# Kernel optimization log

Hardware: AMD Instinct MI355X
Metric: run time of the kernel (lower is better)

The kernel has to match this reference:

```python
import jax, jax.numpy as jnp
import numpy as np

N_NODES, BATCH, VOCAB, HID, OUT = 2047, 128, 32, 128, 128


def setup_inputs() -> dict:
    key = jax.random.key(0)
    ks = jax.random.split(key, 18)
    w = 0.05  # small init scale (xavier-ish for these sizes)
    rn = lambda k, s, sc=w: jax.random.normal(k, s, dtype=jnp.float32) * sc
    return {
        "targets": jax.random.normal(ks[0], (N_NODES, BATCH, VOCAB), dtype=jnp.float32),
        "masks": jnp.ones((N_NODES, BATCH), dtype=jnp.float32),
        "wir_w": rn(ks[1], (HID, VOCAB)), "wir_b": rn(ks[2], (HID,)),
        "whr_w": rn(ks[3], (HID, 2 * HID)), "whr_b": rn(ks[4], (HID,)),
        "wiz_w": rn(ks[5], (HID, VOCAB)), "wiz_b": rn(ks[6], (HID,)),
        "whz_w": rn(ks[7], (HID, 2 * HID)), "whz_b": rn(ks[8], (HID,)),
        "win_w": rn(ks[9], (HID, VOCAB)), "win_b": rn(ks[10], (HID,)),
        "whn_w": rn(ks[11], (HID, 2 * HID)), "whn_b": rn(ks[12], (HID,)),
        "mu_w": rn(ks[13], (OUT, HID)), "mu_b": rn(ks[14], (OUT,)),
        "lv_w": rn(ks[15], (OUT, HID)), "lv_b": rn(ks[16], (OUT,)),
    }


def _encode(targets, masks, wir_w, wir_b, whr_w, whr_b, wiz_w, wiz_b,
            whz_w, whz_b, win_w, win_b, whn_w, whn_b):
    # Complete binary tree in heap layout: level d occupies nodes [2^d-1, 2^(d+1)-1).
    # Bottom-up level sweep == the original node-by-node recursion, but each
    # level's GRU221 cells are batched into one fused GEMM group.
    Nn, B, V = targets.shape
    H = wir_w.shape[0]
    D = int(np.log2(Nn + 1))  # static at trace time
    h_prev = None  # hidden states of the level below, [2^(d+1)*B, H]
    for d in range(D - 1, -1, -1):
        n = 1 << d
        start = n - 1
        x = targets[start:start + n].reshape(n * B, V)
        m = masks[start:start + n].reshape(n * B, 1)
        if h_prev is None:  # leaves: zero children
            h1 = jnp.zeros((n * B, H), dtype=targets.dtype)
            h2 = h1
        else:
            hp = h_prev.reshape(2 * n, B, H)
            h1 = hp[0::2].reshape(n * B, H)  # left children (heap idx 2i+1)
            h2 = hp[1::2].reshape(n * B, H)  # right children (heap idx 2i+2)
        h = jnp.concatenate([h1, h2], axis=1)  # [nB, 2H]
        r = jax.nn.sigmoid(x @ wir_w.T + wir_b + h @ whr_w.T + whr_b)
        z = jax.nn.sigmoid(x @ wiz_w.T + wiz_b + h @ whz_w.T + whz_b)
        c = jnp.tanh(x @ win_w.T + win_b + r * (h @ whn_w.T + whn_b))
        h_out = (1 - z) * c + z * 0.5 * h1 + z * 0.5 * h2
        h_prev = h_out * m
    return h_prev  # root hidden, [B, H]


def reference(targets, masks, wir_w, wir_b, whr_w, whr_b, wiz_w, wiz_b,
              whz_w, whz_b, win_w, win_b, whn_w, whn_b,
              mu_w, mu_b, lv_w, lv_b):
    root = _encode(targets, masks, wir_w, wir_b, whr_w, whr_b,
                   wiz_w, wiz_b, whz_w, whz_b, win_w, win_b, whn_w, whn_b)
    mu = root @ mu_w.T + mu_b
    logvar = root @ lv_w.T + lv_b
    return mu, logvar
```

## Files before the change

### kernel.cpp

```cpp
#include <hip/hip_runtime.h>
#include <hip/hip_bf16.h>
#include <math.h>

#define B 128
#define V 32
#define H 128
#define LDH 264
#define NTHR 256

typedef __attribute__((ext_vector_type(8))) short bf16x8;
typedef __attribute__((ext_vector_type(4))) float f32x4;

__device__ inline f32x4 mfma_bf16(bf16x8 a, bf16x8 b, f32x4 c) {
    return __builtin_amdgcn_mfma_f32_16x16x32_bf16(a, b, c, 0, 0, 0);
}
__device__ inline unsigned short f2bf(float f) {
    __hip_bfloat16 h = __float2bfloat16(f);
    return __builtin_bit_cast(unsigned short, h);
}
__device__ inline float bf2f(unsigned short u) {
    unsigned int x = ((unsigned int)u) << 16;
    return __builtin_bit_cast(float, x);
}
__device__ inline float fast_sigmoid(float x) {
    float e = __builtin_amdgcn_exp2f(x * -1.44269504f);
    return __builtin_amdgcn_rcpf(1.f + e);
}
__device__ inline float fast_tanh(float x) {
    float e = __builtin_amdgcn_exp2f(x * 2.88539008f);
    return 1.f - 2.f * __builtin_amdgcn_rcpf(e + 1.f);
}
__device__ inline bf16x8 load_xfrag(const float* p) {
    float4 a = *(const float4*)p;
    float4 b = *(const float4*)(p + 4);
    bf16x8 r;
    r[0] = (short)f2bf(a.x); r[1] = (short)f2bf(a.y);
    r[2] = (short)f2bf(a.z); r[3] = (short)f2bf(a.w);
    r[4] = (short)f2bf(b.x); r[5] = (short)f2bf(b.y);
    r[6] = (short)f2bf(b.z); r[7] = (short)f2bf(b.w);
    return r;
}

__global__ void prep_pack(const float* __restrict__ wir_w, const float* __restrict__ whr_w,
                          const float* __restrict__ wiz_w, const float* __restrict__ whz_w,
                          const float* __restrict__ win_w, const float* __restrict__ whn_w,
                          const float* __restrict__ wir_b, const float* __restrict__ whr_b,
                          const float* __restrict__ wiz_b, const float* __restrict__ whz_b,
                          const float* __restrict__ win_b, const float* __restrict__ whn_b,
                          const float* __restrict__ mu_w, const float* __restrict__ mu_b,
                          const float* __restrict__ lv_w, const float* __restrict__ lv_b,
                          unsigned short* __restrict__ wFrag, unsigned short* __restrict__ pFrag,
                          float* __restrict__ bias)
{
    int idx = blockIdx.x * blockDim.x + threadIdx.x;
    if (idx < 13824) {
        int lane = idx & 63;
        int ctks = idx >> 6;
        int ct = ctks % 24;
        int ks = ctks / 24;
        int g = ct >> 3;
        int t = ct & 7;
        int u = t * 16 + (lane & 15);
        const float* wi = (g == 0) ? wir_w : (g == 1) ? wiz_w : win_w;
        const float* wh = (g == 0) ? whr_w : (g == 1) ? whz_w : whn_w;
        unsigned short v[8] __attribute__((aligned(16)));
        #pragma unroll
        for (int i = 0; i < 8; ++i) {
            float f;
            if (ks == 0) { int k = 8 * (lane >> 4) + i; f = wi[u * V + k]; }
            else         { int k = (ks - 1) * 32 + 8 * (lane >> 4) + i; f = wh[u * 256 + k]; }
            v[i] = f2bf(f);
        }
        *(int4*)(wFrag + (size_t)idx * 8) = *(const int4*)v;
    } else if (idx < 13824 + 4096) {
        int pidx = idx - 13824;
        int lane = pidx & 63;
        int rest = pidx >> 6;
        int ct2 = rest & 15;
        int ks = rest >> 4;
        int sel = ct2 >> 3, tl = ct2 & 7;
        int u = tl * 16 + (lane & 15);
        const float* wsrc = sel ? lv_w : mu_w;
        unsigned short v[8] __attribute__((aligned(16)));
        #pragma unroll
        for (int i = 0; i < 8; ++i) {
            int k = ks * 32 + 8 * (lane >> 4) + i;
            v[i] = f2bf(wsrc[u * H + k]);
        }
        *(int4*)(pFrag + (size_t)pidx * 8) = *(const int4*)v;
    }
    if (idx < 6 * H) {
        int s = idx / H, u = idx % H;
        float val;
        if (s == 0)      val = wir_b[u] + whr_b[u];
        else if (s == 1) val = wiz_b[u] + whz_b[u];
        else if (s == 2) val = win_b[u];
        else if (s == 3) val = whn_b[u];
        else if (s == 4) val = mu_b[u];
        else             val = lv_b[u];
        bias[idx] = val;
    }
}

__global__ __launch_bounds__(NTHR, 4) void leaf_d9_kernel(
    const float* __restrict__ targets, const float* __restrict__ masks,
    unsigned short* __restrict__ lvl9,
    const unsigned short* __restrict__ wFrag, const float* __restrict__ bias)
{
    __shared__ __attribute__((aligned(16))) unsigned short h_lds[32 * LDH];

    const int tid = threadIdx.x;
    const int lane = tid & 63;
    const int w = tid >> 6;
    const int l15 = lane & 15;
    const int lg = lane >> 4;
    const int j = blockIdx.x >> 2;
    const int q = blockIdx.x & 3;

    const size_t r9 = (size_t)(511 + j) * B + (size_t)q * 32;
    bf16x8 x9_0 = load_xfrag(targets + (r9 + l15) * V + 8 * lg);
    bf16x8 x9_1 = load_xfrag(targets + (r9 + 16 + l15) * V + 8 * lg);

    #pragma unroll
    for (int c = 0; c < 2; ++c) {
        const size_t crow = (size_t)(1023 + 2 * j + c) * B + (size_t)q * 32;
        bf16x8 xf0 = load_xfrag(targets + (crow + l15) * V + 8 * lg);
        bf16x8 xf1 = load_xfrag(targets + (crow + 16 + l15) * V + 8 * lg);
        f32x4 z4 = {0.f, 0.f, 0.f, 0.f};
        f32x4 ar[2][2], az[2][2], an[2][2];
        #pragma unroll
        for (int rt = 0; rt < 2; ++rt)
            #pragma unroll
            for (int t = 0; t < 2; ++t) { ar[rt][t] = z4; az[rt][t] = z4; an[rt][t] = z4; }
        #pragma unroll
        for (int t = 0; t < 2; ++t) {
            int tt = 2 * w + t;
            bf16x8 br_ = *(const bf16x8*)(wFrag + ((size_t)(tt) * 64 + lane) * 8);
            bf16x8 bz_ = *(const bf16x8*)(wFrag + ((size_t)(8 + tt) * 64 + lane) * 8);
            bf16x8 bn_ = *(const bf16x8*)(wFrag + ((size_t)(16 + tt) * 64 + lane) * 8);
            ar[0][t] = mfma_bf16(xf0, br_, ar[0][t]);
            ar[1][t] = mfma_bf16(xf1, br_, ar[1][t]);
            az[0][t] = mfma_bf16(xf0, bz_, az[0][t]);
            az[1][t] = mfma_bf16(xf1, bz_, az[1][t]);
            an[0][t] = mfma_bf16(xf0, bn_, an[0][t]);
            an[1][t] = mfma_bf16(xf1, bn_, an[1][t]);
        }
        #pragma unroll
        for (int t = 0; t < 2; ++t) {
            int u = w * 32 + t * 16 + l15;
            float br = bias[u], bz = bias[128 + u], bin = bias[256 + u], bhn = bias[384 + u];
            #pragma unroll
            for (int rt = 0; rt < 2; ++rt) {
                float4 mv = *(const float4*)(masks + crow + rt * 16 + lg * 4);
                const float* mp = (const float*)&mv;
                #pragma unroll
                for (int reg = 0; reg < 4; ++reg) {
                    int row = rt * 16 + lg * 4 + reg;
                    float rg = fast_sigmoid(ar[rt][t][reg] + br);
                    float zg = fast_sigmoid(az[rt][t][reg] + bz);
                    float cg = fast_tanh(an[rt][t][reg] + bin + rg * bhn);
                    float ho = (1.f - zg) * cg;
                    h_lds[row * LDH + c * 128 + u] = f2bf(ho * mp[reg]);
                }
            }
        }
    }
    __syncthreads();

    f32x4 z4 = {0.f, 0.f, 0.f, 0.f};
    f32x4 acc_r[2][2], acc_z[2][2], acc_in[2][2], acc_hn[2][2];
    #pragma unroll
    for (int rt = 0; rt < 2; ++rt)
        #pragma unroll
        for (int t = 0; t < 2; ++t) {
            acc_r[rt][t] = z4; acc_z[rt][t] = z4; acc_in[rt][t] = z4; acc_hn[rt][t] = z4;
        }
    #pragma unroll
    for (int t = 0; t < 2; ++t) {
        int tt = 2 * w + t;
        bf16x8 br_ = *(const bf16x8*)(wFrag + ((size_t)(tt) * 64 + lane) * 8);
        bf16x8 bz_ = *(const bf16x8*)(wFrag + ((size_t)(8 + tt) * 64 + lane) * 8);
        bf16x8 bn_ = *(const bf16x8*)(wFrag + ((size_t)(16 + tt) * 64 + lane) * 8);
        acc_r[0][t] = mfma_bf16(x9_0, br_, acc_r[0][t]);
        acc_r[1][t] = mfma_bf16(x9_1, br_, acc_r[1][t]);
        acc_z[0][t] = mfma_bf16(x9_0, bz_, acc_z[0][t]);
        acc_z[1][t] = mfma_bf16(x9_1, bz_, acc_z[1][t]);
        acc_in[0][t] = mfma_bf16(x9_0, bn_, acc_in[0][t]);
        acc_in[1][t] = mfma_bf16(x9_1, bn_, acc_in[1][t]);
    }
    #pragma unroll 2
    for (int ks = 1; ks <= 8; ++ks) {
        bf16x8 a0 = *(const bf16x8*)(&h_lds[l15 * LDH + (ks - 1) * 32 + 8 * lg]);
        bf16x8 a1 = *(const bf16x8*)(&h_lds[(16 + l15) * LDH + (ks - 1) * 32 + 8 * lg]);
        size_t fb = (size_t)ks * 24 * 64;
        #pragma unroll
        for (int t = 0; t < 2; ++t) {
            int tt = 2 * w + t;
            bf16x8 br_ = *(const bf16x8*)(wFrag + (fb + (size_t)(tt) * 64 + lane) * 8);
            bf16x8 bz_ = *(const bf16x8*)(wFrag + (fb + (size_t)(8 + tt) * 64 + lane) * 8);
            bf16x8 bn_ = *(const bf16x8*)(wFrag + (fb + (size_t)(16 + tt) * 64 + lane) * 8);
            acc_r[0][t] = mfma_bf16(a0, br_, acc_r[0][t]);
            acc_r[1][t] = mfma_bf16(a1, br_, acc_r[1][t]);
            acc_z[0][t] = mfma_bf16(a0, bz_, acc_z[0][t]);
            acc_z[1][t] = mfma_bf16(a1, bz_, acc_z[1][t]);
            acc_hn[0][t] = mfma_bf16(a0, bn_, acc_hn[0][t]);
            acc_hn[1][t] = mfma_bf16(a1, bn_, acc_hn[1][t]);
        }
    }
    #pragma unroll
    for (int t = 0; t < 2; ++t) {
        int u = w * 32 + t * 16 + l15;
        float br = bias[u], bz = bias[128 + u], bin = bias[256 + u], bhn = bias[384 + u];
        #pragma unroll
        for (int rt = 0; rt < 2; ++rt) {
            float4 mv = *(const float4*)(masks + r9 + rt * 16 + lg * 4);
            const float* mp = (const float*)&mv;
            #pragma unroll
            for (int reg = 0; reg < 4; ++reg) {
                int row = rt * 16 + lg * 4 + reg;
                float rg = fast_sigmoid(acc_r[rt][t][reg] + br);
                float zg = fast_sigmoid(acc_z[rt][t][reg] + bz);
                float cg = fast_tanh(acc_in[rt][t][reg] + bin + rg * (acc_hn[rt][t][reg] + bhn));
                float h1 = bf2f(h_lds[row * LDH + u]);
                float h2 = bf2f(h_lds[row * LDH + 128 + u]);
                float ho = (1.f - zg) * cg + zg * 0.5f * (h1 + h2);
                lvl9[((size_t)j * B + (size_t)q * 32 + row) * H + u] = f2bf(ho * mp[reg]);
            }
        }
    }
}

__global__ __launch_bounds__(NTHR, 4) void level_kernel(
    const float* __restrict__ targets, const float* __restrict__ masks,
    int start,
    const unsigned short* __restrict__ prev, unsigned short* __restrict__ outb,
    const unsigned short* __restrict__ wFrag, const float* __restrict__ bias)
{
    __shared__ __attribute__((aligned(16))) unsigned short h_lds[32 * LDH];

    const int tid = threadIdx.x;
    const int lane = tid & 63;
    const int w = tid >> 6;
// ... 1 lines not shown
    const int lg = lane >> 4;
    const int n = blockIdx.x >> 2;
    const int q = blockIdx.x & 3;

    #pragma unroll
    for (int t = 0; t < 4; ++t) {
        int task = t * NTHR + tid;
        int row = task >> 5;
        int ck = task & 31;
        int4 v = *(const int4*)(prev + (((size_t)(2 * n + (ck >> 4))) * B + (size_t)q * 32 + row) * H + (ck & 15) * 8);
        *(int4*)(&h_lds[row * LDH + ck * 8]) = v;
    }
    const size_t rx = (size_t)(start + n) * B + (size_t)q * 32;
    bf16x8 x0 = load_xfrag(targets + (rx + l15) * V + 8 * lg);
    bf16x8 x1 = load_xfrag(targets + (rx + 16 + l15) * V + 8 * lg);
    __syncthreads();

    f32x4 z4 = {0.f, 0.f, 0.f, 0.f};
    f32x4 acc_r[2][2], acc_z[2][2], acc_in[2][2], acc_hn[2][2];
    #pragma unroll
    for (int rt = 0; rt < 2; ++rt)
        #pragma unroll
        for (int t = 0; t < 2; ++t) {
            acc_r[rt][t] = z4; acc_z[rt][t] = z4; acc_in[rt][t] = z4; acc_hn[rt][t] = z4;
        }
    #pragma unroll
    for (int t = 0; t < 2; ++t) {
        int tt = 2 * w + t;
        bf16x8 br_ = *(const bf16x8*)(wFrag + ((size_t)(tt) * 64 + lane) * 8);
        bf16x8 bz_ = *(const bf16x8*)(wFrag + ((size_t)(8 + tt) * 64 + lane) * 8);
        bf16x8 bn_ = *(const bf16x8*)(wFrag + ((size_t)(16 + tt) * 64 + lane) * 8);
        acc_r[0][t] = mfma_bf16(x0, br_, acc_r[0][t]);
        acc_r[1][t] = mfma_bf16(x1, br_, acc_r[1][t]);
        acc_z[0][t] = mfma_bf16(x0, bz_, acc_z[0][t]);
        acc_z[1][t] = mfma_bf16(x1, bz_, acc_z[1][t]);
        acc_in[0][t] = mfma_bf16(x0, bn_, acc_in[0][t]);
        acc_in[1][t] = mfma_bf16(x1, bn_, acc_in[1][t]);
    }
    #pragma unroll 2
    for (int ks = 1; ks <= 8; ++ks) {
        bf16x8 a0 = *(const bf16x8*)(&h_lds[l15 * LDH + (ks - 1) * 32 + 8 * lg]);
        bf16x8 a1 = *(const bf16x8*)(&h_lds[(16 + l15) * LDH + (ks - 1) * 32 + 8 * lg]);
        size_t fb = (size_t)ks * 24 * 64;
        #pragma unroll
        for (int t = 0; t < 2; ++t) {
            int tt = 2 * w + t;
            bf16x8 br_ = *(const bf16x8*)(wFrag + (fb + (size_t)(tt) * 64 + lane) * 8);
            bf16x8 bz_ = *(const bf16x8*)(wFrag + (fb + (size_t)(8 + tt) * 64 + lane) * 8);
            bf16x8 bn_ = *(const bf16x8*)(wFrag + (fb + (size_t)(16 + tt) * 64 + lane) * 8);
            acc_r[0][t] = mfma_bf16(a0, br_, acc_r[0][t]);
            acc_r[1][t] = mfma_bf16(a1, br_, acc_r[1][t]);
            acc_z[0][t] = mfma_bf16(a0, bz_, acc_z[0][t]);
            acc_z[1][t] = mfma_bf16(a1, bz_, acc_z[1][t]);
            acc_hn[0][t] = mfma_bf16(a0, bn_, acc_hn[0][t]);
            acc_hn[1][t] = mfma_bf16(a1, bn_, acc_hn[1][t]);
        }
    }
    #pragma unroll
    for (int t = 0; t < 2; ++t) {
        int u = w * 32 + t * 16 + l15;
        float br = bias[u], bz = bias[128 + u], bin = bias[256 + u], bhn = bias[384 + u];
        #pragma unroll
        for (int rt = 0; rt < 2; ++rt) {
            float4 mv = *(const float4*)(masks + rx + rt * 16 + lg * 4);
            const float* mp = (const float*)&mv;
            #pragma unroll
            for (int reg = 0; reg < 4; ++reg) {
                int row = rt * 16 + lg * 4 + reg;
                float rg = fast_sigmoid(acc_r[rt][t][reg] + br);
                float zg = fast_sigmoid(acc_z[rt][t][reg] + bz);
                float cg = fast_tanh(acc_in[rt][t][reg] + bin + rg * (acc_hn[rt][t][reg] + bhn));
                float h1 = bf2f(h_lds[row * LDH + u]);
                float h2 = bf2f(h_lds[row * LDH + 128 + u]);
                float ho = (1.f - zg) * cg + zg * 0.5f * (h1 + h2);
                outb[((size_t)n * B + (size_t)q * 32 + row) * H + u] = f2bf(ho * mp[reg]);
            }
        }
    }
}

__global__ __launch_bounds__(NTHR, 4) void pair_kernel(
    const float* __restrict__ targets, const float* __restrict__ masks,
    int du,
    const unsigned short* __restrict__ prev,
    unsigned short* __restrict__ outl,
    const unsigned short* __restrict__ wFrag, const float* __restrict__ bias,
    int do_proj, const unsigned short* __restrict__ pFrag, float* __restrict__ proj_out)
{
    __shared__ __attribute__((aligned(16))) unsigned short hc[32 * LDH];
    __shared__ __attribute__((aligned(16))) unsigned short hp[16 * LDH];

// ... 8 lines not shown

    #pragma unroll
    for (int t = 0; t < 4; ++t) {
        int task = t * NTHR + tid;
        int row = task >> 5;
        int ck = task & 31;
        int gnode = 4 * p + ((row >> 4) << 1) + (ck >> 4);
        int4 v = *(const int4*)(prev + (((size_t)gnode) * B + (size_t)c8 * 16 + (row & 15)) * H + (ck & 15) * 8);
        *(int4*)(&hc[row * LDH + ck * 8]) = v;
    }
    const size_t cbase = (size_t)((1 << du) - 1) + 2 * p;
    bf16x8 xc0 = load_xfrag(targets + ((cbase) * B + (size_t)c8 * 16 + l15) * V + 8 * lg);
    bf16x8 xc1 = load_xfrag(targets + ((cbase + 1) * B + (size_t)c8 * 16 + l15) * V + 8 * lg);
    const size_t pnode = (size_t)((1 << dl) - 1) + p;
    bf16x8 xp = load_xfrag(targets + (pnode * B + (size_t)c8 * 16 + l15) * V + 8 * lg);
    __syncthreads();

    {
        f32x4 z4 = {0.f, 0.f, 0.f, 0.f};
        f32x4 acc_r[2][2], acc_z[2][2], acc_in[2][2], acc_hn[2][2];
        #pragma unroll
        for (int rt = 0; rt < 2; ++rt)
            #pragma unroll
            for (int t = 0; t < 2; ++t) {
                acc_r[rt][t] = z4; acc_z[rt][t] = z4; acc_in[rt][t] = z4; acc_hn[rt][t] = z4;
            }
        #pragma unroll
        for (int t = 0; t < 2; ++t) {
            int tt = 2 * w + t;
            bf16x8 br_ = *(const bf16x8*)(wFrag + ((size_t)(tt) * 64 + lane) * 8);
            bf16x8 bz_ = *(const bf16x8*)(wFrag + ((size_t)(8 + tt) * 64 + lane) * 8);
            bf16x8 bn_ = *(const bf16x8*)(wFrag + ((size_t)(16 + tt) * 64 + lane) * 8);
            acc_r[0][t] = mfma_bf16(xc0, br_, acc_r[0][t]);
            acc_r[1][t] = mfma_bf16(xc1, br_, acc_r[1][t]);
            acc_z[0][t] = mfma_bf16(xc0, bz_, acc_z[0][t]);
            acc_z[1][t] = mfma_bf16(xc1, bz_, acc_z[1][t]);
            acc_in[0][t] = mfma_bf16(xc0, bn_, acc_in[0][t]);
            acc_in[1][t] = mfma_bf16(xc1, bn_, acc_in[1][t]);
        }
        #pragma unroll 2
        for (int ks = 1; ks <= 8; ++ks) {
            bf16x8 a0 = *(const bf16x8*)(&hc[l15 * LDH + (ks - 1) * 32 + 8 * lg]);
            bf16x8 a1 = *(const bf16x8*)(&hc[(16 + l15) * LDH + (ks - 1) * 32 + 8 * lg]);
            size_t fb = (size_t)ks * 24 * 64;
            #pragma unroll
            for (int t = 0; t < 2; ++t) {
                int tt = 2 * w + t;
                bf16x8 br_ = *(const bf16x8*)(wFrag + (fb + (size_t)(tt) * 64 + lane) * 8);
                bf16x8 bz_ = *(const bf16x8*)(wFrag + (fb + (size_t)(8 + tt) * 64 + lane) * 8);
                bf16x8 bn_ = *(const bf16x8*)(wFrag + (fb + (size_t)(16 + tt) * 64 + lane) * 8);
                acc_r[0][t] = mfma_bf16(a0, br_, acc_r[0][t]);
                acc_r[1][t] = mfma_bf16(a1, br_, acc_r[1][t]);
                acc_z[0][t] = mfma_bf16(a0, bz_, acc_z[0][t]);
                acc_z[1][t] = mfma_bf16(a1, bz_, acc_z[1][t]);
                acc_hn[0][t] = mfma_bf16(a0, bn_, acc_hn[0][t]);
                acc_hn[1][t] = mfma_bf16(a1, bn_, acc_hn[1][t]);
            }
        }
        #pragma unroll
        for (int t = 0; t < 2; ++t) {
            int u = w * 32 + t * 16 + l15;
            float br = bias[u], bz = bias[128 + u], bin = bias[256 + u], bhn = bias[384 + u];
            #pragma unroll
            for (int rt = 0; rt < 2; ++rt) {
                float4 mv = *(const float4*)(masks + (cbase + rt) * B + (size_t)c8 * 16 + lg * 4);
                const float* mp = (const float*)&mv;
                #pragma unroll
                for (int reg = 0; reg < 4; ++reg) {
                    int rowl = lg * 4 + reg;
                    int row = rt * 16 + rowl;
                    float rg = fast_sigmoid(acc_r[rt][t][reg] + br);
                    float zg = fast_sigmoid(acc_z[rt][t][reg] + bz);
                    float cg = fast_tanh(acc_in[rt][t][reg] + bin + rg * (acc_hn[rt][t][reg] + bhn));
                    float h1 = bf2f(hc[row * LDH + u]);
                    float h2 = bf2f(hc[row * LDH + 128 + u]);
                    float ho = (1.f - zg) * cg + zg * 0.5f * (h1 + h2);
                    hp[rowl * LDH + rt * 128 + u] = f2bf(ho * mp[reg]);
                }
            }
        }
    }
    __syncthreads();

    {
        f32x4 z4 = {0.f, 0.f, 0.f, 0.f};
        f32x4 acc_r[2], acc_z[2], acc_in[2], acc_hn[2];
        #pragma unroll
        for (int t = 0; t < 2; ++t) { acc_r[t] = z4; acc_z[t] = z4; acc_in[t] = z4; acc_hn[t] = z4; }
        #pragma unroll
        for (int t = 0; t < 2; ++t) {
            int tt = 2 * w + t;
            bf16x8 br_ = *(const bf16x8*)(wFrag + ((size_t)(tt) * 64 + lane) * 8);
            bf16x8 bz_ = *(const bf16x8*)(wFrag + ((size_t)(8 + tt) * 64 + lane) * 8);
            bf16x8 bn_ = *(const bf16x8*)(wFrag + ((size_t)(16 + tt) * 64 + lane) * 8);
            acc_r[t] = mfma_bf16(xp, br_, acc_r[t]);
            acc_z[t] = mfma_bf16(xp, bz_, acc_z[t]);
            acc_in[t] = mfma_bf16(xp, bn_, acc_in[t]);
        }
        #pragma unroll 2
        for (int ks = 1; ks <= 8; ++ks) {
            bf16x8 a = *(const bf16x8*)(&hp[l15 * LDH + (ks - 1) * 32 + 8 * lg]);
            size_t fb = (size_t)ks * 24 * 64;
            #pragma unroll
            for (int t = 0; t < 2; ++t) {
                int tt = 2 * w + t;
                bf16x8 br_ = *(const bf16x8*)(wFrag + (fb + (size_t)(tt) * 64 + lane) * 8);
                bf16x8 bz_ = *(const bf16x8*)(wFrag + (fb + (size_t)(8 + tt) * 64 + lane) * 8);
                bf16x8 bn_ = *(const bf16x8*)(wFrag + (fb + (size_t)(16 + tt) * 64 + lane) * 8);
                acc_r[t] = mfma_bf16(a, br_, acc_r[t]);
                acc_z[t] = mfma_bf16(a, bz_, acc_z[t]);
                acc_hn[t] = mfma_bf16(a, bn_, acc_hn[t]);
            }
        }
        #pragma unroll
        for (int t = 0; t < 2; ++t) {
            int u = w * 32 + t * 16 + l15;
            float br = bias[u], bz = bias[128 + u], bin = bias[256 + u], bhn = bias[384 + u];
            float4 mv = *(const float4*)(masks + pnode * B + (size_t)c8 * 16 + lg * 4);
            const float* mp = (const float*)&mv;
            #pragma unroll
            for (int reg = 0; reg < 4; ++reg) {
                int rowl = lg * 4 + reg;
                float rg = fast_sigmoid(acc_r[t][reg] + br);
                float zg = fast_sigmoid(acc_z[t][reg] + bz);
                float cg = fast_tanh(acc_in[t][reg] + bin + rg * (acc_hn[t][reg] + bhn));
                float h1 = bf2f(hp[rowl * LDH + u]);
                float h2 = bf2f(hp[rowl * LDH + 128 + u]);
                float ho = (1.f - zg) * cg + zg * 0.5f * (h1 + h2);
                unsigned short hb = f2bf(ho * mp[reg]);
                outl[((size_t)p * B + (size_t)c8 * 16 + rowl) * H + u] = hb;
                if (do_proj) hp[rowl * LDH + u] = hb;
            }
        }
    }

    if (do_proj) {
        __syncthreads();
        f32x4 z4 = {0.f, 0.f, 0.f, 0.f};
        f32x4 pa[4] = {z4, z4, z4, z4};
        #pragma unroll
        for (int ks = 0; ks < 4; ++ks) {
            bf16x8 a = *(const bf16x8*)(&hp[l15 * LDH + ks * 32 + 8 * lg]);
            #pragma unroll
            for (int jj = 0; jj < 4; ++jj) {
                bf16x8 f = *(const bf16x8*)(pFrag + (((size_t)ks * 16 + 4 * w + jj) * 64 + lane) * 8);
                pa[jj] = mfma_bf16(a, f, pa[jj]);
            }
        }
        #pragma unroll
        for (int jj = 0; jj < 4; ++jj) {
            int ct2 = 4 * w + jj;
            int sel = ct2 >> 3, tl = ct2 & 7;
            int u = tl * 16 + l15;
            float bb = bias[512 + sel * 128 + u];
            #pragma unroll
            for (int reg = 0; reg < 4; ++reg) {
                int row = c8 * 16 + lg * 4 + reg;
                proj_out[((size_t)sel * B + row) * H + u] = pa[jj][reg] + bb;
            }
        }
    }
}

extern "C" void kernel_launch(void* const* d_in, const int* in_sizes, int n_in,
                              void* d_out, int out_size, void* d_ws, size_t ws_size,
                              hipStream_t stream)
{
    const float* targets = (const float*)d_in[0];
    const float* masks   = (const float*)d_in[1];
    const float* wir_w = (const float*)d_in[2];  const float* wir_b = (const float*)d_in[3];
    const float* whr_w = (const float*)d_in[4];  const float* whr_b = (const float*)d_in[5];
    const float* wiz_w = (const float*)d_in[6];  const float* wiz_b = (const float*)d_in[7];
    const float* whz_w = (const float*)d_in[8];  const float* whz_b = (const float*)d_in[9];
    const float* win_w = (const float*)d_in[10]; const float* win_b = (const float*)d_in[11];
// ... 34 lines not shown
```

Measured before the change: 131.6 us.

## Swap MFMA operands so outputs are row-contiguous; fold bias and exp scales into weights

Swaps the A and B operands of every MFMA so each lane's four accumulator registers hold four consecutive hidden units of one batch row. This turns scalar 2-byte LDS and global stores into packed 8-byte stores, and lets biases load as float4 and seed the accumulators. The log2e scaling for sigmoid and tanh is premultiplied into the bf16 weights and biases in the prep kernel, which removes per-element multiplies and bias adds in the gate epilogues. The leaf kernel also hoists its input weight fragments into registers, at the cost of higher register pressure and a slightly different bf16 rounding of the scaled weights.

```diff
diff --git a/kernel.cpp b/kernel.cpp
--- a/kernel.cpp
+++ b/kernel.cpp
@@ -11,8 +11,8 @@
 typedef __attribute__((ext_vector_type(8))) short bf16x8;
 typedef __attribute__((ext_vector_type(4))) float f32x4;
 
-__device__ inline f32x4 mfma_bf16(bf16x8 a, bf16x8 b, f32x4 c) {
-    return __builtin_amdgcn_mfma_f32_16x16x32_bf16(a, b, c, 0, 0, 0);
+__device__ inline f32x4 mfma_wx(bf16x8 wf, bf16x8 xf, f32x4 c) {
+    return __builtin_amdgcn_mfma_f32_16x16x32_bf16(wf, xf, c, 0, 0, 0);
 }
 __device__ inline unsigned short f2bf(float f) {
     __hip_bfloat16 h = __float2bfloat16(f);
@@ -22,13 +22,11 @@
     unsigned int x = ((unsigned int)u) << 16;
     return __builtin_bit_cast(float, x);
 }
-__device__ inline float fast_sigmoid(float x) {
-    float e = __builtin_amdgcn_exp2f(x * -1.44269504f);
-    return __builtin_amdgcn_rcpf(1.f + e);
-}
-__device__ inline float fast_tanh(float x) {
-    float e = __builtin_amdgcn_exp2f(x * 2.88539008f);
-    return 1.f - 2.f * __builtin_amdgcn_rcpf(e + 1.f);
+__device__ inline float sig_pre(float y) {
+    return __builtin_amdgcn_rcpf(1.f + __builtin_amdgcn_exp2f(y));
+}
+__device__ inline float tanh_pre(float y) {
+    return 1.f - 2.f * __builtin_amdgcn_rcpf(__builtin_amdgcn_exp2f(y) + 1.f);
 }
 __device__ inline bf16x8 load_xfrag(const float* p) {
     float4 a = *(const float4*)p;
@@ -38,6 +36,12 @@
     r[2] = (short)f2bf(a.z); r[3] = (short)f2bf(a.w);
     r[4] = (short)f2bf(b.x); r[5] = (short)f2bf(b.y);
     r[6] = (short)f2bf(b.z); r[7] = (short)f2bf(b.w);
+    return r;
+}
+__device__ inline uint2 pack4(float a, float b, float c, float d) {
+    uint2 r;
+    r.x = (unsigned int)f2bf(a) | ((unsigned int)f2bf(b) << 16);
+    r.y = (unsigned int)f2bf(c) | ((unsigned int)f2bf(d) << 16);
     return r;
 }
 
@@ -61,6 +65,7 @@
         int g = ct >> 3;
         int t = ct & 7;
         int u = t * 16 + (lane & 15);
+        const float scl = (g == 2) ? 2.88539008f : -1.44269504f;
         const float* wi = (g == 0) ? wir_w : (g == 1) ? wiz_w : win_w;
         const float* wh = (g == 0) ? whr_w : (g == 1) ? whz_w : whn_w;
         unsigned short v[8] __attribute__((aligned(16)));
@@ -69,7 +74,7 @@
             float f;
             if (ks == 0) { int k = 8 * (lane >> 4) + i; f = wi[u * V + k]; }
             else         { int k = (ks - 1) * 32 + 8 * (lane >> 4) + i; f = wh[u * 256 + k]; }
-            v[i] = f2bf(f);
+            v[i] = f2bf(f * scl);
         }
         *(int4*)(wFrag + (size_t)idx * 8) = *(const int4*)v;
     } else if (idx < 13824 + 4096) {
@@ -92,10 +97,10 @@
     if (idx < 6 * H) {
         int s = idx / H, u = idx % H;
         float val;
-        if (s == 0)      val = wir_b[u] + whr_b[u];
-        else if (s == 1) val = wiz_b[u] + whz_b[u];
-        else if (s == 2) val = win_b[u];
-        else if (s == 3) val = whn_b[u];
+        if (s == 0)      val = (wir_b[u] + whr_b[u]) * -1.44269504f;
+        else if (s == 1) val = (wiz_b[u] + whz_b[u]) * -1.44269504f;
+        else if (s == 2) val = win_b[u] * 2.88539008f;
+        else if (s == 3) val = whn_b[u] * 2.88539008f;
         else if (s == 4) val = mu_b[u];
         else             val = lv_b[u];
         bias[idx] = val;
@@ -117,6 +122,23 @@
     const int j = blockIdx.x >> 2;
     const int q = blockIdx.x & 3;
 
+    bf16x8 w0[2][3];
+    #pragma unroll
+    for (int t = 0; t < 2; ++t)
+        #pragma unroll
+        for (int g = 0; g < 3; ++g)
+            w0[t][g] = *(const bf16x8*)(wFrag + (((size_t)g * 8 + 2 * w + t) * 64 + lane) * 8);
+
+    f32x4 b_r[2], b_z[2], b_in[2], b_hn[2];
+    #pragma unroll
+    for (int t = 0; t < 2; ++t) {
+        int u0 = w * 32 + t * 16 + lg * 4;
+        b_r[t]  = *(const f32x4*)(bias + u0);
+        b_z[t]  = *(const f32x4*)(bias + 128 + u0);
+        b_in[t] = *(const f32x4*)(bias + 256 + u0);
+        b_hn[t] = *(const f32x4*)(bias + 384 + u0);
+    }
+
     const size_t r9 = (size_t)(511 + j) * B + (size_t)q * 32;
     bf16x8 x9_0 = load_xfrag(targets + (r9 + l15) * V + 8 * lg);
     bf16x8 x9_1 = load_xfrag(targets + (r9 + 16 + l15) * V + 8 * lg);
@@ -126,67 +148,59 @@
         const size_t crow = (size_t)(1023 + 2 * j + c) * B + (size_t)q * 32;
         bf16x8 xf0 = load_xfrag(targets + (crow + l15) * V + 8 * lg);
         bf16x8 xf1 = load_xfrag(targets + (crow + 16 + l15) * V + 8 * lg);
-        f32x4 z4 = {0.f, 0.f, 0.f, 0.f};
         f32x4 ar[2][2], az[2][2], an[2][2];
         #pragma unroll
-        for (int rt = 0; rt < 2; ++rt)
-            #pragma unroll
-            for (int t = 0; t < 2; ++t) { ar[rt][t] = z4; az[rt][t] = z4; an[rt][t] = z4; }
-        #pragma unroll
-        for (int t = 0; t < 2; ++t) {
-            int tt = 2 * w + t;
-            bf16x8 br_ = *(const bf16x8*)(wFrag + ((size_t)(tt) * 64 + lane) * 8);
-            bf16x8 bz_ = *(const bf16x8*)(wFrag + ((size_t)(8 + tt) * 64 + lane) * 8);
-            bf16x8 bn_ = *(const bf16x8*)(wFrag + ((size_t)(16 + tt) * 64 + lane) * 8);
-            ar[0][t] = mfma_bf16(xf0, br_, ar[0][t]);
-            ar[1][t] = mfma_bf16(xf1, br_, ar[1][t]);
-            az[0][t] = mfma_bf16(xf0, bz_, az[0][t]);
-            az[1][t] = mfma_bf16(xf1, bz_, az[1][t]);
-            an[0][t] = mfma_bf16(xf0, bn_, an[0][t]);
-            an[1][t] = mfma_bf16(xf1, bn_, an[1][t]);
-        }
-        #pragma unroll
-        for (int t = 0; t < 2; ++t) {
-            int u = w * 32 + t * 16 + l15;
-            float br = bias[u], bz = bias[128 + u], bin = bias[256 + u], bhn = bias[384 + u];
-            #pragma unroll
-            for (int rt = 0; rt < 2; ++rt) {
-                float4 mv = *(const float4*)(masks + crow + rt * 16 + lg * 4);
-                const float* mp = (const float*)&mv;
+        for (int t = 0; t < 2; ++t) {
+            ar[0][t] = b_r[t];  ar[1][t] = b_r[t];
+            az[0][t] = b_z[t];  az[1][t] = b_z[t];
+            an[0][t] = b_in[t]; an[1][t] = b_in[t];
+        }
+        #pragma unroll
+        for (int t = 0; t < 2; ++t) {
+            ar[0][t] = mfma_wx(w0[t][0], xf0, ar[0][t]);
+            ar[1][t] = mfma_wx(w0[t][0], xf1, ar[1][t]);
+            az[0][t] = mfma_wx(w0[t][1], xf0, az[0][t]);
+            az[1][t] = mfma_wx(w0[t][1], xf1, az[1][t]);
+            an[0][t] = mfma_wx(w0[t][2], xf0, an[0][t]);
+            an[1][t] = mfma_wx(w0[t][2], xf1, an[1][t]);
+        }
+        #pragma unroll
+        for (int rt = 0; rt < 2; ++rt) {
+            int row = rt * 16 + l15;
+            float m = masks[crow + row];
+            #pragma unroll
+            for (int t = 0; t < 2; ++t) {
+                int u0 = w * 32 + t * 16 + lg * 4;
+                float ho[4];
                 #pragma unroll
                 for (int reg = 0; reg < 4; ++reg) {
-                    int row = rt * 16 + lg * 4 + reg;
-                    float rg = fast_sigmoid(ar[rt][t][reg] + br);
-                    float zg = fast_sigmoid(az[rt][t][reg] + bz);
-                    float cg = fast_tanh(an[rt][t][reg] + bin + rg * bhn);
-                    float ho = (1.f - zg) * cg;
-                    h_lds[row * LDH + c * 128 + u] = f2bf(ho * mp[reg]);
+                    float rg = sig_pre(ar[rt][t][reg]);
+                    float zg = sig_pre(az[rt][t][reg]);
+                    float cg = tanh_pre(an[rt][t][reg] + rg * b_hn[t][reg]);
+                    ho[reg] = (cg - zg * cg) * m;
                 }
+                *(uint2*)(&h_lds[row * LDH + c * 128 + u0]) = pack4(ho[0], ho[1], ho[2], ho[3]);
             }
         }
     }
     __syncthreads();
 
-    f32x4 z4 = {0.f, 0.f, 0.f, 0.f};
     f32x4 acc_r[2][2], acc_z[2][2], acc_in[2][2], acc_hn[2][2];
     #pragma unroll
-    for (int rt = 0; rt < 2; ++rt)
-        #pragma unroll
-        for (int t = 0; t < 2; ++t) {
-            acc_r[rt][t] = z4; acc_z[rt][t] = z4; acc_in[rt][t] = z4; acc_hn[rt][t] = z4;
-        }
-    #pragma unroll
-    for (int t = 0; t < 2; ++t) {
-        int tt = 2 * w + t;
-        bf16x8 br_ = *(const bf16x8*)(wFrag + ((size_t)(tt) * 64 + lane) * 8);
-        bf16x8 bz_ = *(const bf16x8*)(wFrag + ((size_t)(8 + tt) * 64 + lane) * 8);
-        bf16x8 bn_ = *(const bf16x8*)(wFrag + ((size_t)(16 + tt) * 64 + lane) * 8);
-        acc_r[0][t] = mfma_bf16(x9_0, br_, acc_r[0][t]);
-        acc_r[1][t] = mfma_bf16(x9_1, br_, acc_r[1][t]);
-        acc_z[0][t] = mfma_bf16(x9_0, bz_, acc_z[0][t]);
-        acc_z[1][t] = mfma_bf16(x9_1, bz_, acc_z[1][t]);
-        acc_in[0][t] = mfma_bf16(x9_0, bn_, acc_in[0][t]);
-        acc_in[1][t] = mfma_bf16(x9_1, bn_, acc_in[1][t]);
+    for (int t = 0; t < 2; ++t) {
+        acc_r[0][t] = b_r[t];   acc_r[1][t] = b_r[t];
+        acc_z[0][t] = b_z[t];   acc_z[1][t] = b_z[t];
+        acc_in[0][t] = b_in[t]; acc_in[1][t] = b_in[t];
+        acc_hn[0][t] = b_hn[t]; acc_hn[1][t] = b_hn[t];
+    }
+    #pragma unroll
+    for (int t = 0; t < 2; ++t) {
+        acc_r[0][t] = mfma_wx(w0[t][0], x9_0, acc_r[0][t]);
+        acc_r[1][t] = mfma_wx(w0[t][0], x9_1, acc_r[1][t]);
+        acc_z[0][t] = mfma_wx(w0[t][1], x9_0, acc_z[0][t]);
+        acc_z[1][t] = mfma_wx(w0[t][1], x9_1, acc_z[1][t]);
+        acc_in[0][t] = mfma_wx(w0[t][2], x9_0, acc_in[0][t]);
+        acc_in[1][t] = mfma_wx(w0[t][2], x9_1, acc_in[1][t]);
     }
     #pragma unroll 2
     for (int ks = 1; ks <= 8; ++ks) {
@@ -196,36 +210,39 @@
         #pragma unroll
         for (int t = 0; t < 2; ++t) {
             int tt = 2 * w + t;
-            bf16x8 br_ = *(const bf16x8*)(wFrag + (fb + (size_t)(tt) * 64 + lane) * 8);
-            bf16x8 bz_ = *(const bf16x8*)(wFrag + (fb + (size_t)(8 + tt) * 64 + lane) * 8);
-            bf16x8 bn_ = *(const bf16x8*)(wFrag + (fb + (size_t)(16 + tt) * 64 + lane) * 8);
-            acc_r[0][t] = mfma_bf16(a0, br_, acc_r[0][t]);
-            acc_r[1][t] = mfma_bf16(a1, br_, acc_r[1][t]);
-            acc_z[0][t] = mfma_bf16(a0, bz_, acc_z[0][t]);
-            acc_z[1][t] = mfma_bf16(a1, bz_, acc_z[1][t]);
-            acc_hn[0][t] = mfma_bf16(a0, bn_, acc_hn[0][t]);
-            acc_hn[1][t] = mfma_bf16(a1, bn_, acc_hn[1][t]);
-        }
-    }
-    #pragma unroll
-    for (int t = 0; t < 2; ++t) {
-        int u = w * 32 + t * 16 + l15;
-        float br = bias[u], bz = bias[128 + u], bin = bias[256 + u], bhn = bias[384 + u];
-        #pragma unroll
-        for (int rt = 0; rt < 2; ++rt) {
-            float4 mv = *(const float4*)(masks + r9 + rt * 16 + lg * 4);
-            const float* mp = (const float*)&mv;
+            bf16x8 wr_ = *(const bf16x8*)(wFrag + (fb + (size_t)(tt) * 64 + lane) * 8);
+            bf16x8 wz_ = *(const bf16x8*)(wFrag + (fb + (size_t)(8 + tt) * 64 + lane) * 8);
+            bf16x8 wn_ = *(const bf16x8*)(wFrag + (fb + (size_t)(16 + tt) * 64 + lane) * 8);
+            acc_r[0][t] = mfma_wx(wr_, a0, acc_r[0][t]);
+            acc_r[1][t] = mfma_wx(wr_, a1, acc_r[1][t]);
+            acc_z[0][t] = mfma_wx(wz_, a0, acc_z[0][t]);
+            acc_z[1][t] = mfma_wx(wz_, a1, acc_z[1][t]);
+            acc_hn[0][t] = mfma_wx(wn_, a0, acc_hn[0][t]);
+            acc_hn[1][t] = mfma_wx(wn_, a1, acc_hn[1][t]);
+        }
+    }
+    #pragma unroll
+    for (int rt = 0; rt < 2; ++rt) {
+        int row = rt * 16 + l15;
+        float m = masks[r9 + row];
+        #pragma unroll
+        for (int t = 0; t < 2; ++t) {
+            int u0 = w * 32 + t * 16 + lg * 4;
+            ushort4 h1v = *(const ushort4*)(&h_lds[row * LDH + u0]);
+            ushort4 h2v = *(const ushort4*)(&h_lds[row * LDH + 128 + u0]);
+            const unsigned short* h1p = (const unsigned short*)&h1v;
+            const unsigned short* h2p = (const unsigned short*)&h2v;
+            float ho[4];
             #pragma unroll
             for (int reg = 0; reg < 4; ++reg) {
-                int row = rt * 16 + lg * 4 + reg;
-                float rg = fast_sigmoid(acc_r[rt][t][reg] + br);
-                float zg = fast_sigmoid(acc_z[rt][t][reg] + bz);
-                float cg = fast_tanh(acc_in[rt][t][reg] + bin + rg * (acc_hn[rt][t][reg] + bhn));
-                float h1 = bf2f(h_lds[row * LDH + u]);
-                float h2 = bf2f(h_lds[row * LDH + 128 + u]);
-                float ho = (1.f - zg) * cg + zg * 0.5f * (h1 + h2);
-                lvl9[((size_t)j * B + (size_t)q * 32 + row) * H + u] = f2bf(ho * mp[reg]);
-            }
+                float rg = sig_pre(acc_r[rt][t][reg]);
+                float zg = sig_pre(acc_z[rt][t][reg]);
+                float cg = tanh_pre(acc_in[rt][t][reg] + rg * acc_hn[rt][t][reg]);
+                float hm = 0.5f * bf2f(h1p[reg]) + 0.5f * bf2f(h2p[reg]);
+                ho[reg] = (cg + zg * (hm - cg)) * m;
+            }
+            *(uint2*)(lvl9 + ((size_t)j * B + (size_t)q * 32 + row) * H + u0) =
+                pack4(ho[0], ho[1], ho[2], ho[3]);
         }
     }
 }
@@ -257,28 +274,38 @@
     const size_t rx = (size_t)(start + n) * B + (size_t)q * 32;
     bf16x8 x0 = load_xfrag(targets + (rx + l15) * V + 8 * lg);
     bf16x8 x1 = load_xfrag(targets + (rx + 16 + l15) * V + 8 * lg);
+
+    f32x4 b_r[2], b_z[2], b_in[2], b_hn[2];
+    #pragma unroll
+    for (int t = 0; t < 2; ++t) {
+        int u0 = w * 32 + t * 16 + lg * 4;
+        b_r[t]  = *(const f32x4*)(bias + u0);
+        b_z[t]  = *(const f32x4*)(bias + 128 + u0);
+        b_in[t] = *(const f32x4*)(bias + 256 + u0);
+        b_hn[t] = *(const f32x4*)(bias + 384 + u0);
+    }
     __syncthreads();
 
-    f32x4 z4 = {0.f, 0.f, 0.f, 0.f};
     f32x4 acc_r[2][2], acc_z[2][2], acc_in[2][2], acc_hn[2][2];
     #pragma unroll
-    for (int rt = 0; rt < 2; ++rt)
-        #pragma unroll
-        for (int t = 0; t < 2; ++t) {
-            acc_r[rt][t] = z4; acc_z[rt][t] = z4; acc_in[rt][t] = z4; acc_hn[rt][t] = z4;
-        }
+    for (int t = 0; t < 2; ++t) {
+        acc_r[0][t] = b_r[t];   acc_r[1][t] = b_r[t];
+        acc_z[0][t] = b_z[t];   acc_z[1][t] = b_z[t];
+        acc_in[0][t] = b_in[t]; acc_in[1][t] = b_in[t];
+        acc_hn[0][t] = b_hn[t]; acc_hn[1][t] = b_hn[t];
+    }
     #pragma unroll
     for (int t = 0; t < 2; ++t) {
         int tt = 2 * w + t;
-        bf16x8 br_ = *(const bf16x8*)(wFrag + ((size_t)(tt) * 64 + lane) * 8);
-        bf16x8 bz_ = *(const bf16x8*)(wFrag + ((size_t)(8 + tt) * 64 + lane) * 8);
-        bf16x8 bn_ = *(const bf16x8*)(wFrag + ((size_t)(16 + tt) * 64 + lane) * 8);
-        acc_r[0][t] = mfma_bf16(x0, br_, acc_r[0][t]);
-        acc_r[1][t] = mfma_bf16(x1, br_, acc_r[1][t]);
-        acc_z[0][t] = mfma_bf16(x0, bz_, acc_z[0][t]);
-        acc_z[1][t] = mfma_bf16(x1, bz_, acc_z[1][t]);
-        acc_in[0][t] = mfma_bf16(x0, bn_, acc_in[0][t]);
-        acc_in[1][t] = mfma_bf16(x1, bn_, acc_in[1][t]);
+        bf16x8 wr_ = *(const bf16x8*)(wFrag + ((size_t)(tt) * 64 + lane) * 8);
+        bf16x8 wz_ = *(const bf16x8*)(wFrag + ((size_t)(8 + tt) * 64 + lane) * 8);
+        bf16x8 wn_ = *(const bf16x8*)(wFrag + ((size_t)(16 + tt) * 64 + lane) * 8);
+        acc_r[0][t] = mfma_wx(wr_, x0, acc_r[0][t]);
+        acc_r[1][t] = mfma_wx(wr_, x1, acc_r[1][t]);
+        acc_z[0][t] = mfma_wx(wz_, x0, acc_z[0][t]);
+        acc_z[1][t] = mfma_wx(wz_, x1, acc_z[1][t]);
+        acc_in[0][t] = mfma_wx(wn_, x0, acc_in[0][t]);
+        acc_in[1][t] = mfma_wx(wn_, x1, acc_in[1][t]);
     }
     #pragma unroll 2
     for (int ks = 1; ks <= 8; ++ks) {
@@ -288,36 +315,39 @@
         #pragma unroll
         for (int t = 0; t < 2; ++t) {
             int tt = 2 * w + t;
-            bf16x8 br_ = *(const bf16x8*)(wFrag + (fb + (size_t)(tt) * 64 + lane) * 8);
-            bf16x8 bz_ = *(const bf16x8*)(wFrag + (fb + (size_t)(8 + tt) * 64 + lane) * 8);
-            bf16x8 bn_ = *(const bf16x8*)(wFrag + (fb + (size_t)(16 + tt) * 64 + lane) * 8);
-            acc_r[0][t] = mfma_bf16(a0, br_, acc_r[0][t]);
-            acc_r[1][t] = mfma_bf16(a1, br_, acc_r[1][t]);
-            acc_z[0][t] = mfma_bf16(a0, bz_, acc_z[0][t]);
-            acc_z[1][t] = mfma_bf16(a1, bz_, acc_z[1][t]);
-            acc_hn[0][t] = mfma_bf16(a0, bn_, acc_hn[0][t]);
-            acc_hn[1][t] = mfma_bf16(a1, bn_, acc_hn[1][t]);
-        }
-    }
-    #pragma unroll
-    for (int t = 0; t < 2; ++t) {
-        int u = w * 32 + t * 16 + l15;
-        float br = bias[u], bz = bias[128 + u], bin = bias[256 + u], bhn = bias[384 + u];
-        #pragma unroll
-        for (int rt = 0; rt < 2; ++rt) {
-            float4 mv = *(const float4*)(masks + rx + rt * 16 + lg * 4);
-            const float* mp = (const float*)&mv;
+            bf16x8 wr_ = *(const bf16x8*)(wFrag + (fb + (size_t)(tt) * 64 + lane) * 8);
+            bf16x8 wz_ = *(const bf16x8*)(wFrag + (fb + (size_t)(8 + tt) * 64 + lane) * 8);
+            bf16x8 wn_ = *(const bf16x8*)(wFrag + (fb + (size_t)(16 + tt) * 64 + lane) * 8);
+            acc_r[0][t] = mfma_wx(wr_, a0, acc_r[0][t]);
+            acc_r[1][t] = mfma_wx(wr_, a1, acc_r[1][t]);
+            acc_z[0][t] = mfma_wx(wz_, a0, acc_z[0][t]);
+            acc_z[1][t] = mfma_wx(wz_, a1, acc_z[1][t]);
+            acc_hn[0][t] = mfma_wx(wn_, a0, acc_hn[0][t]);
+            acc_hn[1][t] = mfma_wx(wn_, a1, acc_hn[1][t]);
+        }
+    }
+    #pragma unroll
+    for (int rt = 0; rt < 2; ++rt) {
+        int row = rt * 16 + l15;
+        float m = masks[rx + row];
+        #pragma unroll
+        for (int t = 0; t < 2; ++t) {
+            int u0 = w * 32 + t * 16 + lg * 4;
+            ushort4 h1v = *(const ushort4*)(&h_lds[row * LDH + u0]);
+            ushort4 h2v = *(const ushort4*)(&h_lds[row * LDH + 128 + u0]);
+            const unsigned short* h1p = (const unsigned short*)&h1v;
+            const unsigned short* h2p = (const unsigned short*)&h2v;
+            float ho[4];
             #pragma unroll
             for (int reg = 0; reg < 4; ++reg) {
-                int row = rt * 16 + lg * 4 + reg;
-                float rg = fast_sigmoid(acc_r[rt][t][reg] + br);
-                float zg = fast_sigmoid(acc_z[rt][t][reg] + bz);
-                float cg = fast_tanh(acc_in[rt][t][reg] + bin + rg * (acc_hn[rt][t][reg] + bhn));
-                float h1 = bf2f(h_lds[row * LDH + u]);
-                float h2 = bf2f(h_lds[row * LDH + 128 + u]);
-                float ho = (1.f - zg) * cg + zg * 0.5f * (h1 + h2);
-                outb[((size_t)n * B + (size_t)q * 32 + row) * H + u] = f2bf(ho * mp[reg]);
-            }
+                float rg = sig_pre(acc_r[rt][t][reg]);
+                float zg = sig_pre(acc_z[rt][t][reg]);
+                float cg = tanh_pre(acc_in[rt][t][reg] + rg * acc_hn[rt][t][reg]);
+                float hm = 0.5f * bf2f(h1p[reg]) + 0.5f * bf2f(h2p[reg]);
+                ho[reg] = (cg + zg * (hm - cg)) * m;
+            }
+            *(uint2*)(outb + ((size_t)n * B + (size_t)q * 32 + row) * H + u0) =
+                pack4(ho[0], ho[1], ho[2], ho[3]);
         }
     }
 }
@@ -356,29 +386,39 @@
     bf16x8 xc1 = load_xfrag(targets + ((cbase + 1) * B + (size_t)c8 * 16 + l15) * V + 8 * lg);
     const size_t pnode = (size_t)((1 << dl) - 1) + p;
     bf16x8 xp = load_xfrag(targets + (pnode * B + (size_t)c8 * 16 + l15) * V + 8 * lg);
+
+    f32x4 b_r[2], b_z[2], b_in[2], b_hn[2];
+    #pragma unroll
+    for (int t = 0; t < 2; ++t) {
+        int u0 = w * 32 + t * 16 + lg * 4;
+        b_r[t]  = *(const f32x4*)(bias + u0);
+        b_z[t]  = *(const f32x4*)(bias + 128 + u0);
+        b_in[t] = *(const f32x4*)(bias + 256 + u0);
+        b_hn[t] = *(const f32x4*)(bias + 384 + u0);
+    }
     __syncthreads();
 
     {
-        f32x4 z4 = {0.f, 0.f, 0.f, 0.f};
         f32x4 acc_r[2][2], acc_z[2][2], acc_in[2][2], acc_hn[2][2];
         #pragma unroll
-        for (int rt = 0; rt < 2; ++rt)
-            #pragma unroll
-            for (int t = 0; t < 2; ++t) {
-                acc_r[rt][t] = z4; acc_z[rt][t] = z4; acc_in[rt][t] = z4; acc_hn[rt][t] = z4;
-            }
+        for (int t = 0; t < 2; ++t) {
+            acc_r[0][t] = b_r[t];   acc_r[1][t] = b_r[t];
+            acc_z[0][t] = b_z[t];   acc_z[1][t] = b_z[t];
+            acc_in[0][t] = b_in[t]; acc_in[1][t] = b_in[t];
+            acc_hn[0][t] = b_hn[t]; acc_hn[1][t] = b_hn[t];
+        }
         #pragma unroll
         for (int t = 0; t < 2; ++t) {
             int tt = 2 * w + t;
-            bf16x8 br_ = *(const bf16x8*)(wFrag + ((size_t)(tt) * 64 + lane) * 8);
-            bf16x8 bz_ = *(const bf16x8*)(wFrag + ((size_t)(8 + tt) * 64 + lane) * 8);
-            bf16x8 bn_ = *(const bf16x8*)(wFrag + ((size_t)(16 + tt) * 64 + lane) * 8);
-            acc_r[0][t] = mfma_bf16(xc0, br_, acc_r[0][t]);
-            acc_r[1][t] = mfma_bf16(xc1, br_, acc_r[1][t]);
-            acc_z[0][t] = mfma_bf16(xc0, bz_, acc_z[0][t]);
-            acc_z[1][t] = mfma_bf16(xc1, bz_, acc_z[1][t]);
-            acc_in[0][t] = mfma_bf16(xc0, bn_, acc_in[0][t]);
-            acc_in[1][t] = mfma_bf16(xc1, bn_, acc_in[1][t]);
+            bf16x8 wr_ = *(const bf16x8*)(wFrag + ((size_t)(tt) * 64 + lane) * 8);
+            bf16x8 wz_ = *(const bf16x8*)(wFrag + ((size_t)(8 + tt) * 64 + lane) * 8);
+            bf16x8 wn_ = *(const bf16x8*)(wFrag + ((size_t)(16 + tt) * 64 + lane) * 8);
+            acc_r[0][t] = mfma_wx(wr_, xc0, acc_r[0][t]);
+            acc_r[1][t] = mfma_wx(wr_, xc1, acc_r[1][t]);
+            acc_z[0][t] = mfma_wx(wz_, xc0, acc_z[0][t]);
+            acc_z[1][t] = mfma_wx(wz_, xc1, acc_z[1][t]);
+            acc_in[0][t] = mfma_wx(wn_, xc0, acc_in[0][t]);
+            acc_in[1][t] = mfma_wx(wn_, xc1, acc_in[1][t]);
         }
         #pragma unroll 2
         for (int ks = 1; ks <= 8; ++ks) {
@@ -388,56 +428,58 @@
             #pragma unroll
             for (int t = 0; t < 2; ++t) {
                 int tt = 2 * w + t;
-                bf16x8 br_ = *(const bf16x8*)(wFrag + (fb + (size_t)(tt) * 64 + lane) * 8);
-                bf16x8 bz_ = *(const bf16x8*)(wFrag + (fb + (size_t)(8 + tt) * 64 + lane) * 8);
-                bf16x8 bn_ = *(const bf16x8*)(wFrag + (fb + (size_t)(16 + tt) * 64 + lane) * 8);
-                acc_r[0][t] = mfma_bf16(a0, br_, acc_r[0][t]);
-                acc_r[1][t] = mfma_bf16(a1, br_, acc_r[1][t]);
-                acc_z[0][t] = mfma_bf16(a0, bz_, acc_z[0][t]);
-                acc_z[1][t] = mfma_bf16(a1, bz_, acc_z[1][t]);
-                acc_hn[0][t] = mfma_bf16(a0, bn_, acc_hn[0][t]);
-                acc_hn[1][t] = mfma_bf16(a1, bn_, acc_hn[1][t]);
-            }
-        }
-        #pragma unroll
-        for (int t = 0; t < 2; ++t) {
-            int u = w * 32 + t * 16 + l15;
-            float br = bias[u], bz = bias[128 + u], bin = bias[256 + u], bhn = bias[384 + u];
-            #pragma unroll
-            for (int rt = 0; rt < 2; ++rt) {
-                float4 mv = *(const float4*)(masks + (cbase + rt) * B + (size_t)c8 * 16 + lg * 4);
-                const float* mp = (const float*)&mv;
+                bf16x8 wr_ = *(const bf16x8*)(wFrag + (fb + (size_t)(tt) * 64 + lane) * 8);
+                bf16x8 wz_ = *(const bf16x8*)(wFrag + (fb + (size_t)(8 + tt) * 64 + lane) * 8);
+                bf16x8 wn_ = *(const bf16x8*)(wFrag + (fb + (size_t)(16 + tt) * 64 + lane) * 8);
+                acc_r[0][t] = mfma_wx(wr_, a0, acc_r[0][t]);
+                acc_r[1][t] = mfma_wx(wr_, a1, acc_r[1][t]);
+                acc_z[0][t] = mfma_wx(wz_, a0, acc_z[0][t]);
+                acc_z[1][t] = mfma_wx(wz_, a1, acc_z[1][t]);
+                acc_hn[0][t] = mfma_wx(wn_, a0, acc_hn[0][t]);
+                acc_hn[1][t] = mfma_wx(wn_, a1, acc_hn[1][t]);
+            }
+        }
+        #pragma unroll
+        for (int rt = 0; rt < 2; ++rt) {
+            float m = masks[(cbase + rt) * B + (size_t)c8 * 16 + l15];
+            int hrow = rt * 16 + l15;
+            #pragma unroll
+            for (int t = 0; t < 2; ++t) {
+                int u0 = w * 32 + t * 16 + lg * 4;
+                ushort4 h1v = *(const ushort4*)(&hc[hrow * LDH + u0]);
+                ushort4 h2v = *(const ushort4*)(&hc[hrow * LDH + 128 + u0]);
+                const unsigned short* h1p = (const unsigned short*)&h1v;
+                const unsigned short* h2p = (const unsigned short*)&h2v;
+                float ho[4];
                 #pragma unroll
                 for (int reg = 0; reg < 4; ++reg) {
-                    int rowl = lg * 4 + reg;
-                    int row = rt * 16 + rowl;
-                    float rg = fast_sigmoid(acc_r[rt][t][reg] + br);
-                    float zg = fast_sigmoid(acc_z[rt][t][reg] + bz);
-                    float cg = fast_tanh(acc_in[rt][t][reg] + bin + rg * (acc_hn[rt][t][reg] + bhn));
-                    float h1 = bf2f(hc[row * LDH + u]);
-                    float h2 = bf2f(hc[row * LDH + 128 + u]);
-                    float ho = (1.f - zg) * cg + zg * 0.5f * (h1 + h2);
-                    hp[rowl * LDH + rt * 128 + u] = f2bf(ho * mp[reg]);
+                    float rg = sig_pre(acc_r[rt][t][reg]);
+                    float zg = sig_pre(acc_z[rt][t][reg]);
+                    float cg = tanh_pre(acc_in[rt][t][reg] + rg * acc_hn[rt][t][reg]);
+                    float hm = 0.5f * bf2f(h1p[reg]) + 0.5f * bf2f(h2p[reg]);
+                    ho[reg] = (cg + zg * (hm - cg)) * m;
                 }
+                *(uint2*)(&hp[l15 * LDH + rt * 128 + u0]) = pack4(ho[0], ho[1], ho[2], ho[3]);
             }
         }
     }
     __syncthreads();
 
     {
-        f32x4 z4 = {0.f, 0.f, 0.f, 0.f};
         f32x4 acc_r[2], acc_z[2], acc_in[2], acc_hn[2];
         #pragma unroll
-        for (int t = 0; t < 2; ++t) { acc_r[t] = z4; acc_z[t] = z4; acc_in[t] = z4; acc_hn[t] = z4; }
+        for (int t = 0; t < 2; ++t) {
+            acc_r[t] = b_r[t]; acc_z[t] = b_z[t]; acc_in[t] = b_in[t]; acc_hn[t] = b_hn[t];
+        }
         #pragma unroll
         for (int t = 0; t < 2; ++t) {
             int tt = 2 * w + t;
-            bf16x8 br_ = *(const bf16x8*)(wFrag + ((size_t)(tt) * 64 + lane) * 8);
-            bf16x8 bz_ = *(const bf16x8*)(wFrag + ((size_t)(8 + tt) * 64 + lane) * 8);
-            bf16x8 bn_ = *(const bf16x8*)(wFrag + ((size_t)(16 + tt) * 64 + lane) * 8);
-            acc_r[t] = mfma_bf16(xp, br_, acc_r[t]);
-            acc_z[t] = mfma_bf16(xp, bz_, acc_z[t]);
-            acc_in[t] = mfma_bf16(xp, bn_, acc_in[t]);
+            bf16x8 wr_ = *(const bf16x8*)(wFrag + ((size_t)(tt) * 64 + lane) * 8);
+            bf16x8 wz_ = *(const bf16x8*)(wFrag + ((size_t)(8 + tt) * 64 + lane) * 8);
+            bf16x8 wn_ = *(const bf16x8*)(wFrag + ((size_t)(16 + tt) * 64 + lane) * 8);
+            acc_r[t] = mfma_wx(wr_, xp, acc_r[t]);
+            acc_z[t] = mfma_wx(wz_, xp, acc_z[t]);
+            acc_in[t] = mfma_wx(wn_, xp, acc_in[t]);
         }
         #pragma unroll 2
         for (int ks = 1; ks <= 8; ++ks) {
@@ -446,60 +488,62 @@
             #pragma unroll
             for (int t = 0; t < 2; ++t) {
                 int tt = 2 * w + t;
-                bf16x8 br_ = *(const bf16x8*)(wFrag + (fb + (size_t)(tt) * 64 + lane) * 8);
-                bf16x8 bz_ = *(const bf16x8*)(wFrag + (fb + (size_t)(8 + tt) * 64 + lane) * 8);
-                bf16x8 bn_ = *(const bf16x8*)(wFrag + (fb + (size_t)(16 + tt) * 64 + lane) * 8);
-                acc_r[t] = mfma_bf16(a, br_, acc_r[t]);
-                acc_z[t] = mfma_bf16(a, bz_, acc_z[t]);
-                acc_hn[t] = mfma_bf16(a, bn_, acc_hn[t]);
-            }
-        }
-        #pragma unroll
-        for (int t = 0; t < 2; ++t) {
-            int u = w * 32 + t * 16 + l15;
-            float br = bias[u], bz = bias[128 + u], bin = bias[256 + u], bhn = bias[384 + u];
-            float4 mv = *(const float4*)(masks + pnode * B + (size_t)c8 * 16 + lg * 4);
-            const float* mp = (const float*)&mv;
+                bf16x8 wr_ = *(const bf16x8*)(wFrag + (fb + (size_t)(tt) * 64 + lane) * 8);
+                bf16x8 wz_ = *(const bf16x8*)(wFrag + (fb + (size_t)(8 + tt) * 64 + lane) * 8);
+                bf16x8 wn_ = *(const bf16x8*)(wFrag + (fb + (size_t)(16 + tt) * 64 + lane) * 8);
+                acc_r[t] = mfma_wx(wr_, a, acc_r[t]);
+                acc_z[t] = mfma_wx(wz_, a, acc_z[t]);
+                acc_hn[t] = mfma_wx(wn_, a, acc_hn[t]);
+            }
+        }
+        float m = masks[pnode * B + (size_t)c8 * 16 + l15];
+        #pragma unroll
+        for (int t = 0; t < 2; ++t) {
+            int u0 = w * 32 + t * 16 + lg * 4;
+            ushort4 h1v = *(const ushort4*)(&hp[l15 * LDH + u0]);
+            ushort4 h2v = *(const ushort4*)(&hp[l15 * LDH + 128 + u0]);
+            const unsigned short* h1p = (const unsigned short*)&h1v;
+            const unsigned short* h2p = (const unsigned short*)&h2v;
+            float ho[4];
             #pragma unroll
             for (int reg = 0; reg < 4; ++reg) {
-                int rowl = lg * 4 + reg;
-                float rg = fast_sigmoid(acc_r[t][reg] + br);
-                float zg = fast_sigmoid(acc_z[t][reg] + bz);
-                float cg = fast_tanh(acc_in[t][reg] + bin + rg * (acc_hn[t][reg] + bhn));
-                float h1 = bf2f(hp[rowl * LDH + u]);
-                float h2 = bf2f(hp[rowl * LDH + 128 + u]);
-                float ho = (1.f - zg) * cg + zg * 0.5f * (h1 + h2);
-                unsigned short hb = f2bf(ho * mp[reg]);
-                outl[((size_t)p * B + (size_t)c8 * 16 + rowl) * H + u] = hb;
-                if (do_proj) hp[rowl * LDH + u] = hb;
-            }
+                float rg = sig_pre(acc_r[t][reg]);
+                float zg = sig_pre(acc_z[t][reg]);
+                float cg = tanh_pre(acc_in[t][reg] + rg * acc_hn[t][reg]);
+                float hm = 0.5f * bf2f(h1p[reg]) + 0.5f * bf2f(h2p[reg]);
+                ho[reg] = (cg + zg * (hm - cg)) * m;
+            }
+            uint2 pk = pack4(ho[0], ho[1], ho[2], ho[3]);
+            *(uint2*)(outl + ((size_t)p * B + (size_t)c8 * 16 + l15) * H + u0) = pk;
+            if (do_proj) *(uint2*)(&hp[l15 * LDH + u0]) = pk;
         }
     }
 
     if (do_proj) {
         __syncthreads();
-        f32x4 z4 = {0.f, 0.f, 0.f, 0.f};
-        f32x4 pa[4] = {z4, z4, z4, z4};
-        #pragma unroll
-        for (int ks = 0; ks < 4; ++ks) {
-            bf16x8 a = *(const bf16x8*)(&hp[l15 * LDH + ks * 32 + 8 * lg]);
-            #pragma unroll
-            for (int jj = 0; jj < 4; ++jj) {
-                bf16x8 f = *(const bf16x8*)(pFrag + (((size_t)ks * 16 + 4 * w + jj) * 64 + lane) * 8);
-                pa[jj] = mfma_bf16(a, f, pa[jj]);
-            }
-        }
+        f32x4 pa[4];
         #pragma unroll
         for (int jj = 0; jj < 4; ++jj) {
             int ct2 = 4 * w + jj;
             int sel = ct2 >> 3, tl = ct2 & 7;
-            int u = tl * 16 + l15;
-            float bb = bias[512 + sel * 128 + u];
-            #pragma unroll
-            for (int reg = 0; reg < 4; ++reg) {
-                int row = c8 * 16 + lg * 4 + reg;
-                proj_out[((size_t)sel * B + row) * H + u] = pa[jj][reg] + bb;
-            }
+            pa[jj] = *(const f32x4*)(bias + 512 + sel * 128 + tl * 16 + lg * 4);
+        }
+        #pragma unroll
+        for (int ks = 0; ks < 4; ++ks) {
+            bf16x8 a = *(const bf16x8*)(&hp[l15 * LDH + ks * 32 + 8 * lg]);
+            #pragma unroll
+            for (int jj = 0; jj < 4; ++jj) {
+                bf16x8 f = *(const bf16x8*)(pFrag + (((size_t)ks * 16 + 4 * w + jj) * 64 + lane) * 8);
+                pa[jj] = mfma_wx(f, a, pa[jj]);
+            }
+        }
+        #pragma unroll
+        for (int jj = 0; jj < 4; ++jj) {
+            int ct2 = 4 * w + jj;
+            int sel = ct2 >> 3, tl = ct2 & 7;
+            int u0 = tl * 16 + lg * 4;
+            int row = c8 * 16 + l15;
+            *(f32x4*)(proj_out + ((size_t)sel * B + row) * H + u0) = pa[jj];
         }
     }
 }
```

Result: slower. 136.1 us (+3.5%).
